# Optimization experiments

Hardware: AMD Instinct MI355X
Metric: run time of the kernel (lower is better)

## Reference

```python
import jax, jax.numpy as jnp
import numpy as np

EPS = 1e-5
DIM = 1024
HEADS = 8
DIM_HEAD = 64
INNER = HEADS * DIM_HEAD  # 512


def layernorm(x, g, b):
    mu = jnp.mean(x, axis=-1, keepdims=True)
    var = jnp.var(x, axis=-1, keepdims=True)
    return (x - mu) * jax.lax.rsqrt(var + EPS) * g + b


def setup_inputs() -> dict:
    key = jax.random.key(0)
    ks = jax.random.split(key, 5)
    b, t, n, m = 4, 4, 2048, 64
    x = jax.random.normal(ks[0], (b, t, n, DIM), dtype=jnp.float32)
    latents = jax.random.normal(ks[1], (b, t, m, DIM), dtype=jnp.float32)
    Wq = jax.random.normal(ks[2], (DIM, INNER), dtype=jnp.float32) * (DIM ** -0.5)
    Wkv = jax.random.normal(ks[3], (DIM, 2 * INNER), dtype=jnp.float32) * (DIM ** -0.5)
    Wo = jax.random.normal(ks[4], (INNER, DIM), dtype=jnp.float32) * (INNER ** -0.5)
    return {
        "x": x, "latents": latents,
        "g_x": jnp.ones((DIM,), jnp.float32), "b_x": jnp.zeros((DIM,), jnp.float32),
        "g_l": jnp.ones((DIM,), jnp.float32), "b_l": jnp.zeros((DIM,), jnp.float32),
        "Wq": Wq, "Wkv": Wkv, "Wo": Wo,
    }


def reference(x, latents, g_x, b_x, g_l, b_l, Wq, Wkv, Wo):
    b, t, n, d = x.shape
    m = latents.shape[2]
    h, dh = HEADS, DIM_HEAD
    scale = dh ** -0.5

    xn = layernorm(x, g_x, b_x)              # (b,t,n,d)
    ln = layernorm(latents, g_l, b_l)        # (b,t,m,d)

    q = jnp.einsum('btmd,de->btme', ln, Wq)  # (b,t,m,inner)
    kv_in = jnp.concatenate([xn, ln], axis=-2)           # (b,t,n+m,d)
    kv = jnp.einsum('btjd,de->btje', kv_in, Wkv)         # (b,t,n+m,2*inner)
    k, v = jnp.split(kv, 2, axis=-1)

    q = q.reshape(b, t, m, h, dh) * scale
    k = k.reshape(b, t, n + m, h, dh)
    v = v.reshape(b, t, n + m, h, dh)

    sim = jnp.einsum('btihd,btjhd->bhtij', q, k)         # (b,h,t,m,n+m)
    sim = sim - jax.lax.stop_gradient(jnp.max(sim, axis=-1, keepdims=True))
    attn = jax.nn.softmax(sim, axis=-1)
    out = jnp.einsum('bhtij,btjhd->btihd', attn, v)      # (b,t,m,h,dh)
    out = out.reshape(b, t, m, h * dh)
    return jnp.einsum('btme,ed->btmd', out, Wo)          # (b,t,m,d)
```

## Files before the change

kernel.cpp:

```cpp
#include <hip/hip_runtime.h>
#include <cstdint>
#include <cstddef>

typedef __attribute__((ext_vector_type(8))) short short8;
typedef __attribute__((ext_vector_type(4))) short short4v;
typedef __attribute__((ext_vector_type(4))) float f32x4;

__device__ __forceinline__ short f2bf(float f) {
    union { float f; unsigned u; } c; c.f = f;
    unsigned r = c.u + 0x7fffu + ((c.u >> 16) & 1u);
    return (short)(r >> 16);
}

__global__ __launch_bounds__(256) void conv_weights(
    const float* __restrict__ Wq, const float* __restrict__ Wkv, const float* __restrict__ Wo,
    short* __restrict__ WqT, short* __restrict__ WkvT, short* __restrict__ WoT)
{
    int idx = blockIdx.x * 256 + threadIdx.x;
    if (idx < 1024 * 1024) {
        int n = idx >> 10, k = idx & 1023;
        WkvT[idx] = f2bf(Wkv[k * 1024 + n]);
    } else if (idx < 1024 * 1024 + 512 * 1024) {
        int j = idx - 1024 * 1024;
        int n = j >> 10, k = j & 1023;
        WqT[j] = f2bf(Wq[k * 512 + n] * 0.125f);
    } else {
        int j = idx - (1024 * 1024 + 512 * 1024);
        int n = j >> 9, k = j & 511;
        WoT[j] = f2bf(Wo[k * 1024 + n]);
    }
}

__global__ __launch_bounds__(256) void ln_kernel(
    const float* __restrict__ x, const float* __restrict__ lat,
    const float* __restrict__ gx, const float* __restrict__ bx,
    const float* __restrict__ gl, const float* __restrict__ bl,
    short* __restrict__ Aout, short* __restrict__ Lq)
{
    const int blk = blockIdx.x;
    const int tid = threadIdx.x;
    const float *src, *g, *b; size_t drow; short* dst2 = nullptr;
    if (blk < 32768) {
        int bt = blk >> 11, i = blk & 2047;
        src = x + (size_t)blk * 1024; g = gx; b = bx;
        drow = (size_t)bt * 2112 + i;
    } else {
        int idx = blk - 32768;
        int bt = idx >> 6, i = idx & 63;
        src = lat + (size_t)idx * 1024; g = gl; b = bl;
        drow = (size_t)bt * 2112 + 2048 + i;
        dst2 = Lq + (size_t)idx * 1024;
    }
    float4 v = ((const float4*)src)[tid];
    float s  = v.x + v.y + v.z + v.w;
    float s2 = v.x * v.x + v.y * v.y + v.z * v.z + v.w * v.w;
    for (int off = 32; off >= 1; off >>= 1) { s += __shfl_down(s, off); s2 += __shfl_down(s2, off); }
    __shared__ float red[8];
    const int wv = tid >> 6, ln_ = tid & 63;
    if (ln_ == 0) { red[wv] = s; red[4 + wv] = s2; }
    __syncthreads();
    s  = red[0] + red[1] + red[2] + red[3];
    s2 = red[4] + red[5] + red[6] + red[7];
    const float mu   = s * (1.f / 1024.f);
    const float var  = s2 * (1.f / 1024.f) - mu * mu;
    const float rstd = rsqrtf(var + 1e-5f);
    float4 gv = ((const float4*)g)[tid];
    float4 bv = ((const float4*)b)[tid];
    short4v o;
    o[0] = f2bf((v.x - mu) * rstd * gv.x + bv.x);
    o[1] = f2bf((v.y - mu) * rstd * gv.y + bv.y);
    o[2] = f2bf((v.z - mu) * rstd * gv.z + bv.z);
    o[3] = f2bf((v.w - mu) * rstd * gv.w + bv.w);
    *(short4v*)(Aout + drow * 1024 + tid * 4) = o;
    if (dst2) *(short4v*)(dst2 + tid * 4) = o;
}

template <typename OutT>
__global__ __launch_bounds__(256) void gemm_bt(
    const short* __restrict__ A, const short* __restrict__ Bt,
    OutT* __restrict__ C, int M, int N, int K)
{
    __shared__ short As[128 * 32];
    __shared__ short Bs[128 * 32];
    const int tid  = threadIdx.x;
    const int wave = tid >> 6, lane = tid & 63;
    const int col  = lane & 15, quad = lane >> 4;
    const int m0 = blockIdx.x * 128, n0 = blockIdx.y * 128;
    const int wm = (wave >> 1) * 64, wn = (wave & 1) * 64;
    const int sr = tid >> 2;
    const int sk = (tid & 3) * 8;

    f32x4 acc[4][4];
    for (int i = 0; i < 4; i++) for (int j = 0; j < 4; j++) acc[i][j] = f32x4{0.f, 0.f, 0.f, 0.f};

    const short* Ar0 = A  + (size_t)(m0 + sr)      * K + sk;
    const short* Ar1 = A  + (size_t)(m0 + sr + 64) * K + sk;
    const short* Br0 = Bt + (size_t)(n0 + sr)      * K + sk;
    const short* Br1 = Bt + (size_t)(n0 + sr + 64) * K + sk;

    for (int k0 = 0; k0 < K; k0 += 32) {
        __syncthreads();
        *(short8*)&As[sr * 32 + sk]        = *(const short8*)(Ar0 + k0);
        *(short8*)&As[(sr + 64) * 32 + sk] = *(const short8*)(Ar1 + k0);
        *(short8*)&Bs[sr * 32 + sk]        = *(const short8*)(Br0 + k0);
        *(short8*)&Bs[(sr + 64) * 32 + sk] = *(const short8*)(Br1 + k0);
        __syncthreads();
        short8 af[4], bf[4];
        for (int mt = 0; mt < 4; mt++) af[mt] = *(const short8*)&As[(wm + mt * 16 + col) * 32 + quad * 8];
        for (int nt = 0; nt < 4; nt++) bf[nt] = *(const short8*)&Bs[(wn + nt * 16 + col) * 32 + quad * 8];
        for (int mt = 0; mt < 4; mt++)
            for (int nt = 0; nt < 4; nt++)
                acc[mt][nt] = __builtin_amdgcn_mfma_f32_16x16x32_bf16(af[mt], bf[nt], acc[mt][nt], 0, 0, 0);
    }
    for (int mt = 0; mt < 4; mt++)
        for (int nt = 0; nt < 4; nt++)
            for (int r = 0; r < 4; r++) {
                int row = m0 + wm + mt * 16 + quad * 4 + r;
                int cc  = n0 + wn + nt * 16 + col;
                float v = acc[mt][nt][r];
                if constexpr (sizeof(OutT) == 2) C[(size_t)row * N + cc] = (OutT)f2bf(v);
                else                             C[(size_t)row * N + cc] = v;
            }
}

__global__ __launch_bounds__(256) void transpose_v(const short* __restrict__ KV, short* __restrict__ Vt)
{
    __shared__ short tile[32][33];
    const int bth = blockIdx.z, bt = bth >> 3, h = bth & 7;
    const int jt = blockIdx.x * 32, dt = blockIdx.y * 32;
    const int x = threadIdx.x, y = threadIdx.y;
    for (int yy = y; yy < 32; yy += 8)
        tile[yy][x] = KV[(size_t)(bt * 2112 + jt + yy) * 1024 + 512 + h * 64 + dt + x];
    __syncthreads();
    for (int yy = y; yy < 32; yy += 8)
        Vt[(size_t)(bth * 64 + dt + yy) * 2112 + jt + x] = tile[x][yy];
}

__global__ __launch_bounds__(256) void attn_kernel(
    const short* __restrict__ Q,
    const short* __restrict__ KV,
    const short* __restrict__ Vt,
    short* __restrict__ AttO)
{
    __shared__ short p_lds[4][64 * 72];
    __shared__ float sm[4][64];
    __shared__ float sl[4][64];
    __shared__ float oacc[64 * 64];

    const int wg = blockIdx.x;
    const int bt = wg >> 3, h = wg & 7;
    const int tid = threadIdx.x;
    const int wave = tid >> 6, lane = tid & 63;
    const int col = lane & 15, quad = lane >> 4;

    short8 qf[4][2];
    for (int mt = 0; mt < 4; mt++)
        for (int ks = 0; ks < 2; ks++)
            qf[mt][ks] = *(const short8*)(Q + (size_t)(bt * 64 + mt * 16 + col) * 512
                                            + h * 64 + ks * 32 + quad * 8);

    float m_run[4][4], l_run[4][4];
    f32x4 o_acc[4][4];
    for (int mt = 0; mt < 4; mt++)
        for (int r = 0; r < 4; r++) { m_run[mt][r] = -__builtin_inff(); l_run[mt][r] = 0.f; }
    for (int mt = 0; mt < 4; mt++)
        for (int dt = 0; dt < 4; dt++) o_acc[mt][dt] = f32x4{0.f, 0.f, 0.f, 0.f};

    short* pl = p_lds[wave];

    for (int jb = wave; jb < 33; jb += 4) {
        f32x4 s[4][4];
        for (int mt = 0; mt < 4; mt++) for (int nt = 0; nt < 4; nt++) s[mt][nt] = f32x4{0.f, 0.f, 0.f, 0.f};
        for (int nt = 0; nt < 4; nt++) {
            const int j = jb * 64 + nt * 16 + col;
            const short* kp = KV + (size_t)(bt * 2112 + j) * 1024 + h * 64 + quad * 8;
            short8 k0 = *(const short8*)kp;
            short8 k1 = *(const short8*)(kp + 32);
            for (int mt = 0; mt < 4; mt++) {
                s[mt][nt] = __builtin_amdgcn_mfma_f32_16x16x32_bf16(qf[mt][0], k0, s[mt][nt], 0, 0, 0);
                s[mt][nt] = __builtin_amdgcn_mfma_f32_16x16x32_bf16(qf[mt][1], k1, s[mt][nt], 0, 0, 0);
            }
        }
        for (int mt = 0; mt < 4; mt++)
            for (int r = 0; r < 4; r++) {
                float mx = fmaxf(fmaxf(s[mt][0][r], s[mt][1][r]), fmaxf(s[mt][2][r], s[mt][3][r]));
                for (int off = 8; off >= 1; off >>= 1) mx = fmaxf(mx, __shfl_xor(mx, off));
                float mnew = fmaxf(m_run[mt][r], mx);
                float alpha = __expf(m_run[mt][r] - mnew);
                float rs = 0.f;
                for (int nt = 0; nt < 4; nt++) {
                    float p = __expf(s[mt][nt][r] - mnew);
                    s[mt][nt][r] = p;
                    rs += p;
                }
                for (int off = 8; off >= 1; off >>= 1) rs += __shfl_xor(rs, off);
                m_run[mt][r] = mnew;
                l_run[mt][r] = l_run[mt][r] * alpha + rs;
                for (int dt = 0; dt < 4; dt++) o_acc[mt][dt][r] *= alpha;
            }
        for (int mt = 0; mt < 4; mt++)
            for (int nt = 0; nt < 4; nt++)
                for (int r = 0; r < 4; r++)
                    pl[(mt * 16 + quad * 4 + r) * 72 + nt * 16 + col] = f2bf(s[mt][nt][r]);
        for (int ks = 0; ks < 2; ks++) {
            short8 vf[4];
            for (int dt = 0; dt < 4; dt++)
                vf[dt] = *(const short8*)(Vt + (size_t)(wg * 64 + dt * 16 + col) * 2112
                                             + jb * 64 + ks * 32 + quad * 8);
            for (int mt = 0; mt < 4; mt++) {
                short8 pf = *(const short8*)(pl + (mt * 16 + col) * 72 + ks * 32 + quad * 8);
                for (int dt = 0; dt < 4; dt++)
                    o_acc[mt][dt] = __builtin_amdgcn_mfma_f32_16x16x32_bf16(pf, vf[dt], o_acc[mt][dt], 0, 0, 0);
            }
        }
    }

    if (col == 0)
        for (int mt = 0; mt < 4; mt++)
            for (int r = 0; r < 4; r++) {
                int row = mt * 16 + quad * 4 + r;
                sm[wave][row] = m_run[mt][r];
                sl[wave][row] = l_run[mt][r];
            }
    __syncthreads();
    for (int mt = 0; mt < 4; mt++)
        for (int r = 0; r < 4; r++) {
            int row = mt * 16 + quad * 4 + r;
            float M = fmaxf(fmaxf(sm[0][row], sm[1][row]), fmaxf(sm[2][row], sm[3][row]));
            float L = sl[0][row] * __expf(sm[0][row] - M) + sl[1][row] * __expf(sm[1][row] - M)
                    + sl[2][row] * __expf(sm[2][row] - M) + sl[3][row] * __expf(sm[3][row] - M);
            float sc = __expf(m_run[mt][r] - M) / L;
            for (int dt = 0; dt < 4; dt++) o_acc[mt][dt][r] *= sc;
        }
    for (int i = tid; i < 64 * 64; i += 256) oacc[i] = 0.f;
    __syncthreads();
    for (int w = 0; w < 4; w++) {
        if (wave == w)
            for (int mt = 0; mt < 4; mt++)
                for (int dt = 0; dt < 4; dt++)
                    for (int r = 0; r < 4; r++)
                        oacc[(mt * 16 + quad * 4 + r) * 64 + dt * 16 + col] += o_acc[mt][dt][r];
        __syncthreads();
    }
    for (int i = tid; i < 64 * 64; i += 256) {
        int row = i >> 6, c = i & 63;
        AttO[(size_t)(bt * 64 + row) * 512 + h * 64 + c] = f2bf(oacc[i]);
    }
}

extern "C" void kernel_launch(void* const* d_in, const int* in_sizes, int n_in,
                              void* d_out, int out_size, void* d_ws, size_t ws_size,
                              hipStream_t stream)
{
    const float* x   = (const float*)d_in[0];
    const float* lat = (const float*)d_in[1];
    const float* g_x = (const float*)d_in[2];
    const float* b_x = (const float*)d_in[3];
    const float* g_l = (const float*)d_in[4];
    const float* b_l = (const float*)d_in[5];
    const float* Wq  = (const float*)d_in[6];
    const float* Wkv = (const float*)d_in[7];
    const float* Wo  = (const float*)d_in[8];
    float* out = (float*)d_out;

    char* ws = (char*)d_ws;
    size_t off = 0;
    auto alloc = [&](size_t bytes) { char* p = ws + off; off += (bytes + 255) & ~(size_t)255; return p; };
    short* A_kvin = (short*)alloc(33792ull * 1024 * 2);
    short* Lq     = (short*)alloc(1024ull * 1024 * 2);
    short* WkvT   = (short*)alloc(1024ull * 1024 * 2);
    short* WqT    = (short*)alloc(512ull * 1024 * 2);
    short* WoT    = (short*)alloc(1024ull * 512 * 2);
    short* KVb    = (short*)alloc(33792ull * 1024 * 2);
    short* Qb     = (short*)alloc(1024ull * 512 * 2);
    short* AttO   = (short*)alloc(1024ull * 512 * 2);
    short* Vt     = A_kvin;

    conv_weights<<<8192, 256, 0, stream>>>(Wq, Wkv, Wo, WqT, WkvT, WoT);
    ln_kernel<<<33792, 256, 0, stream>>>(x, lat, g_x, b_x, g_l, b_l, A_kvin, Lq);
    gemm_bt<short><<<dim3(264, 8), 256, 0, stream>>>(A_kvin, WkvT, KVb, 33792, 1024, 1024);
    gemm_bt<short><<<dim3(8, 4), 256, 0, stream>>>(Lq, WqT, Qb, 1024, 512, 1024);
    transpose_v<<<dim3(66, 2, 128), dim3(32, 8), 0, stream>>>(KVb, Vt);
    attn_kernel<<<128, 256, 0, stream>>>(Qb, KVb, Vt, AttO);
    gemm_bt<float><<<dim3(8, 8), 256, 0, stream>>>(AttO, WoT, out, 1024, 1024, 512);
}
```

Baseline: 449.0 us.

## Split attention over KV chunks with merge kernel, tiled weight transpose, direct-to-LDS GEMM loads

Attention now runs on 128x4 workgroups, each covering a quarter of the KV blocks and writing partial outputs plus row max and sum. A new merge kernel combines these with a log-sum-exp rescale, which raises attention parallelism beyond 128 workgroups on a GPU with many CUs. The weight conversion is rewritten as LDS-tiled transposes for coalesced reads, and the V transpose uses 64-wide vectorized tiles. The GEMM stages tiles through global_load_lds instead of register round-trips. In exchange it adds an extra launch and fp32 partial-result traffic.

Result: faster. 420.0 us (-6.5%).

```diff
diff --git a/kernel.cpp b/kernel.cpp
--- a/kernel.cpp
+++ b/kernel.cpp
@@ -12,23 +12,23 @@
     return (short)(r >> 16);
 }
 
-__global__ __launch_bounds__(256) void conv_weights(
-    const float* __restrict__ Wq, const float* __restrict__ Wkv, const float* __restrict__ Wo,
-    short* __restrict__ WqT, short* __restrict__ WkvT, short* __restrict__ WoT)
-{
-    int idx = blockIdx.x * 256 + threadIdx.x;
-    if (idx < 1024 * 1024) {
-        int n = idx >> 10, k = idx & 1023;
-        WkvT[idx] = f2bf(Wkv[k * 1024 + n]);
-    } else if (idx < 1024 * 1024 + 512 * 1024) {
-        int j = idx - 1024 * 1024;
-        int n = j >> 10, k = j & 1023;
-        WqT[j] = f2bf(Wq[k * 512 + n] * 0.125f);
-    } else {
-        int j = idx - (1024 * 1024 + 512 * 1024);
-        int n = j >> 9, k = j & 511;
-        WoT[j] = f2bf(Wo[k * 1024 + n]);
-    }
+__device__ __forceinline__ void gl2lds16(const void* g, void* l) {
+    __builtin_amdgcn_global_load_lds(
+        (const __attribute__((address_space(1))) void*)g,
+        (__attribute__((address_space(3))) void*)l, 16, 0, 0);
+}
+
+__global__ __launch_bounds__(256) void wconv(
+    const float* __restrict__ S, short* __restrict__ D, int K, int N, float scale)
+{
+    __shared__ float t[32][33];
+    const int kt = blockIdx.x * 32, nt = blockIdx.y * 32;
+    const int x = threadIdx.x & 31, y4 = (threadIdx.x >> 5) * 4;
+    for (int i = 0; i < 4; i++)
+        t[y4 + i][x] = S[(size_t)(kt + y4 + i) * N + nt + x];
+    __syncthreads();
+    for (int i = 0; i < 4; i++)
+        D[(size_t)(nt + y4 + i) * K + kt + x] = f2bf(t[x][y4 + i] * scale);
 }
 
 __global__ __launch_bounds__(256) void ln_kernel(
@@ -97,13 +97,17 @@
     const short* Ar1 = A  + (size_t)(m0 + sr + 64) * K + sk;
     const short* Br0 = Bt + (size_t)(n0 + sr)      * K + sk;
     const short* Br1 = Bt + (size_t)(n0 + sr + 64) * K + sk;
+    short* lA0 = &As[sr * 32 + sk];
+    short* lA1 = &As[(sr + 64) * 32 + sk];
+    short* lB0 = &Bs[sr * 32 + sk];
+    short* lB1 = &Bs[(sr + 64) * 32 + sk];
 
     for (int k0 = 0; k0 < K; k0 += 32) {
         __syncthreads();
-        *(short8*)&As[sr * 32 + sk]        = *(const short8*)(Ar0 + k0);
-        *(short8*)&As[(sr + 64) * 32 + sk] = *(const short8*)(Ar1 + k0);
-        *(short8*)&Bs[sr * 32 + sk]        = *(const short8*)(Br0 + k0);
-        *(short8*)&Bs[(sr + 64) * 32 + sk] = *(const short8*)(Br1 + k0);
+        gl2lds16(Ar0 + k0, lA0);
+        gl2lds16(Ar1 + k0, lA1);
+        gl2lds16(Br0 + k0, lB0);
+        gl2lds16(Br1 + k0, lB1);
         __syncthreads();
         short8 af[4], bf[4];
         for (int mt = 0; mt < 4; mt++) af[mt] = *(const short8*)&As[(wm + mt * 16 + col) * 32 + quad * 8];
@@ -125,22 +129,35 @@
 
 __global__ __launch_bounds__(256) void transpose_v(const short* __restrict__ KV, short* __restrict__ Vt)
 {
-    __shared__ short tile[32][33];
-    const int bth = blockIdx.z, bt = bth >> 3, h = bth & 7;
-    const int jt = blockIdx.x * 32, dt = blockIdx.y * 32;
-    const int x = threadIdx.x, y = threadIdx.y;
-    for (int yy = y; yy < 32; yy += 8)
-        tile[yy][x] = KV[(size_t)(bt * 2112 + jt + yy) * 1024 + 512 + h * 64 + dt + x];
-    __syncthreads();
-    for (int yy = y; yy < 32; yy += 8)
-        Vt[(size_t)(bth * 64 + dt + yy) * 2112 + jt + x] = tile[x][yy];
+    __shared__ short tile[64 * 68];
+    const int bth = blockIdx.y, bt = bth >> 3, h = bth & 7;
+    const int jt = blockIdx.x * 64;
+    const int tid = threadIdx.x;
+    for (int it = 0; it < 2; ++it) {
+        int s = tid + it * 256;
+        int j = s >> 3, dv = (s & 7) * 8;
+        short8 v = *(const short8*)(KV + (size_t)(bt * 2112 + jt + j) * 1024 + 512 + h * 64 + dv);
+        short4v lo = {v[0], v[1], v[2], v[3]}, hi = {v[4], v[5], v[6], v[7]};
+        *(short4v*)&tile[j * 68 + dv]     = lo;
+        *(short4v*)&tile[j * 68 + dv + 4] = hi;
+    }
+    __syncthreads();
+    for (int it = 0; it < 2; ++it) {
+        int s = tid + it * 256;
+        int d = s >> 3, jv = (s & 7) * 8;
+        short8 o;
+        for (int jj = 0; jj < 8; jj++) o[jj] = tile[(jv + jj) * 68 + d];
+        *(short8*)(Vt + (size_t)(bth * 64 + d) * 2112 + jt + jv) = o;
+    }
 }
 
 __global__ __launch_bounds__(256) void attn_kernel(
     const short* __restrict__ Q,
     const short* __restrict__ KV,
     const short* __restrict__ Vt,
-    short* __restrict__ AttO)
+    float* __restrict__ Opart,
+    float* __restrict__ Mp,
+    float* __restrict__ Lp)
 {
     __shared__ short p_lds[4][64 * 72];
     __shared__ float sm[4][64];
@@ -148,6 +165,8 @@
     __shared__ float oacc[64 * 64];
 
     const int wg = blockIdx.x;
+    const int ck = blockIdx.y;
+    const int wgc = wg * 4 + ck;
     const int bt = wg >> 3, h = wg & 7;
     const int tid = threadIdx.x;
     const int wave = tid >> 6, lane = tid & 63;
@@ -168,7 +187,7 @@
 
     short* pl = p_lds[wave];
 
-    for (int jb = wave; jb < 33; jb += 4) {
+    for (int jb = ck * 4 + wave; jb < 33; jb += 16) {
         f32x4 s[4][4];
         for (int mt = 0; mt < 4; mt++) for (int nt = 0; nt < 4; nt++) s[mt][nt] = f32x4{0.f, 0.f, 0.f, 0.f};
         for (int nt = 0; nt < 4; nt++) {
@@ -229,7 +248,8 @@
             float M = fmaxf(fmaxf(sm[0][row], sm[1][row]), fmaxf(sm[2][row], sm[3][row]));
             float L = sl[0][row] * __expf(sm[0][row] - M) + sl[1][row] * __expf(sm[1][row] - M)
                     + sl[2][row] * __expf(sm[2][row] - M) + sl[3][row] * __expf(sm[3][row] - M);
-            float sc = __expf(m_run[mt][r] - M) / L;
+            if (wave == 0 && col == 0) { Mp[wgc * 64 + row] = M; Lp[wgc * 64 + row] = L; }
+            float sc = __expf(m_run[mt][r] - M);
             for (int dt = 0; dt < 4; dt++) o_acc[mt][dt][r] *= sc;
         }
     for (int i = tid; i < 64 * 64; i += 256) oacc[i] = 0.f;
@@ -242,10 +262,26 @@
                         oacc[(mt * 16 + quad * 4 + r) * 64 + dt * 16 + col] += o_acc[mt][dt][r];
         __syncthreads();
     }
-    for (int i = tid; i < 64 * 64; i += 256) {
-        int row = i >> 6, c = i & 63;
-        AttO[(size_t)(bt * 64 + row) * 512 + h * 64 + c] = f2bf(oacc[i]);
-    }
+    for (int i = tid; i < 64 * 64; i += 256)
+        Opart[(size_t)wgc * 4096 + i] = oacc[i];
+}
+
+__global__ __launch_bounds__(256) void attn_merge(
+    const float* __restrict__ Opart, const float* __restrict__ Mp,
+    const float* __restrict__ Lp, short* __restrict__ AttO)
+{
+    int idx = blockIdx.x * 256 + threadIdx.x;
+    int wg = idx >> 12, rd = idx & 4095, row = rd >> 6, d = rd & 63;
+    float M = -__builtin_inff();
+    for (int c = 0; c < 4; c++) M = fmaxf(M, Mp[(wg * 4 + c) * 64 + row]);
+    float L = 0.f, O = 0.f;
+    for (int c = 0; c < 4; c++) {
+        float e = __expf(Mp[(wg * 4 + c) * 64 + row] - M);
+        L += e * Lp[(wg * 4 + c) * 64 + row];
+        O += e * Opart[(size_t)(wg * 4 + c) * 4096 + rd];
+    }
+    int bt = wg >> 3, h = wg & 7;
+    AttO[(size_t)(bt * 64 + row) * 512 + h * 64 + d] = f2bf(O / L);
 }
 
 extern "C" void kernel_launch(void* const* d_in, const int* in_sizes, int n_in,
@@ -274,13 +310,20 @@
     short* KVb    = (short*)alloc(33792ull * 1024 * 2);
     short* Qb     = (short*)alloc(1024ull * 512 * 2);
     short* AttO   = (short*)alloc(1024ull * 512 * 2);
-    short* Vt     = A_kvin;
-
-    conv_weights<<<8192, 256, 0, stream>>>(Wq, Wkv, Wo, WqT, WkvT, WoT);
+    short* Vt    = A_kvin;
+    char*  sc2   = (char*)A_kvin + 36ull * 1024 * 1024;
+    float* Opart = (float*)sc2;
+    float* Mp    = (float*)(sc2 + 8388608);
+    float* Lp    = (float*)(sc2 + 8388608 + 131072);
+
+    wconv<<<dim3(32, 32), 256, 0, stream>>>(Wkv, WkvT, 1024, 1024, 1.0f);
+    wconv<<<dim3(32, 16), 256, 0, stream>>>(Wq,  WqT,  1024, 512,  0.125f);
+    wconv<<<dim3(16, 32), 256, 0, stream>>>(Wo,  WoT,  512,  1024, 1.0f);
     ln_kernel<<<33792, 256, 0, stream>>>(x, lat, g_x, b_x, g_l, b_l, A_kvin, Lq);
     gemm_bt<short><<<dim3(264, 8), 256, 0, stream>>>(A_kvin, WkvT, KVb, 33792, 1024, 1024);
     gemm_bt<short><<<dim3(8, 4), 256, 0, stream>>>(Lq, WqT, Qb, 1024, 512, 1024);
-    transpose_v<<<dim3(66, 2, 128), dim3(32, 8), 0, stream>>>(KVb, Vt);
-    attn_kernel<<<128, 256, 0, stream>>>(Qb, KVb, Vt, AttO);
+    transpose_v<<<dim3(33, 128), 256, 0, stream>>>(KVb, Vt);
+    attn_kernel<<<dim3(128, 4), 256, 0, stream>>>(Qb, KVb, Vt, Opart, Mp, Lp);
+    attn_merge<<<2048, 256, 0, stream>>>(Opart, Mp, Lp, AttO);
     gemm_bt<float><<<dim3(8, 8), 256, 0, stream>>>(AttO, WoT, out, 1024, 1024, 512);
 }
```
